# Optimization experiments

Hardware: AMD Instinct MI355X
Metric: run time of the kernel (lower is better)

The kernel has to match this reference:

```python
import jax, jax.numpy as jnp
import numpy as np

EPS = 1e-5

def layer_norm(x, w, b):
    mu = jnp.mean(x, axis=-1, keepdims=True)
    var = jnp.mean(jnp.square(x - mu), axis=-1, keepdims=True)
    return (x - mu) * jax.lax.rsqrt(var + EPS) * w + b

def setup_inputs() -> dict:
    key = jax.random.key(0)
    ks = jax.random.split(key, 12)
    B, T, C = 4, 2048, 1024
    s = lambda d: 1.0 / np.sqrt(d)
    return {
        "x":      jax.random.normal(ks[0], (B, T, C), dtype=jnp.float32),
        "w_attn": jax.random.normal(ks[1], (C, 3 * C), dtype=jnp.float32) * s(C),
        "b_attn": jnp.zeros((3 * C,), jnp.float32),
        "w_o":    jax.random.normal(ks[2], (C, C), dtype=jnp.float32) * s(C),
        "b_o":    jnp.zeros((C,), jnp.float32),
        "ln_w":   jnp.ones((C,), jnp.float32),
        "ln_b":   jnp.zeros((C,), jnp.float32),
        "w_fc1":  jax.random.normal(ks[3], (C, 4 * C), dtype=jnp.float32) * s(C),
        "b_fc1":  jnp.zeros((4 * C,), jnp.float32),
        "w_fc2":  jax.random.normal(ks[4], (4 * C, C), dtype=jnp.float32) * s(4 * C),
        "b_fc2":  jnp.zeros((C,), jnp.float32),
        "n_heads": 16,
    }

def reference(x, w_attn, b_attn, w_o, b_o, ln_w, ln_b, w_fc1, b_fc1, w_fc2, b_fc2, n_heads):
    B, T, C = x.shape
    H = n_heads
    Dh = C // H
    qkv = x @ w_attn + b_attn                      # [B,T,3C]
    q, k, v = jnp.split(qkv, 3, axis=-1)
    q = q.reshape(B, T, H, Dh).transpose(0, 2, 1, 3)  # [B,H,T,Dh]
    k = k.reshape(B, T, H, Dh).transpose(0, 2, 1, 3)
    v = v.reshape(B, T, H, Dh).transpose(0, 2, 1, 3)
    scores = jnp.einsum("bhtd,bhsd->bhts", q, k) / jnp.sqrt(jnp.float32(Dh))
    w = jax.nn.softmax(scores, axis=-1)            # no causal mask in source
    out = jnp.einsum("bhts,bhsd->bhtd", w, v)      # [B,H,T,Dh]
    out = out.transpose(0, 2, 1, 3).reshape(B, T, C)
    attn_out = out @ w_o + b_o
    x = x + attn_out
    h = layer_norm(x, ln_w, ln_b)
    h = jax.nn.gelu(h @ w_fc1 + b_fc1, approximate=False)
    h = h @ w_fc2 + b_fc2
    return x + h
```

## Files before the change

### kernel.cpp

```cpp
#include <hip/hip_runtime.h>
#include <hip/hip_bf16.h>
#include <math.h>
#include <stdint.h>

typedef __attribute__((ext_vector_type(8))) short s16x8;
typedef __attribute__((ext_vector_type(4))) float f32x4;
typedef __attribute__((ext_vector_type(4))) u_int32_t u32x4;
typedef unsigned int u32;
typedef unsigned short u16;

#define DEVINL __device__ __forceinline__
#define VMW(n) asm volatile("s_waitcnt vmcnt(" #n ")" ::: "memory")

DEVINL u16 f2bf(float f) {
    u32 b = __builtin_bit_cast(u32, f);
    u32 r = (b + 0x7fffu + ((b >> 16) & 1u)) >> 16;
    return (u16)r;
}

DEVINL float fexp2(float x) {
    float r;
    asm("v_exp_f32 %0, %1" : "=v"(r) : "v"(x));
    return r;
}

DEVINL u32 cvt_pk_bf16(float lo, float hi) {
    u32 r;
    asm("v_cvt_pk_bf16_f32 %0, %1, %2" : "=v"(r) : "v"(lo), "v"(hi));
    return r;
}

DEVINL void gload_lds16(const void* g, const void* l) {
    __builtin_amdgcn_global_load_lds(
        (const __attribute__((address_space(1))) u32*)(uintptr_t)g,
        (__attribute__((address_space(3))) u32*)(uintptr_t)l, 16, 0, 0);
}

__global__ __launch_bounds__(256)
void cvt_bf16_kernel(const float* __restrict__ in, u16* __restrict__ out, int n4)
{
    int i = blockIdx.x * 256 + threadIdx.x;
    const int stride = gridDim.x * 256;
    for (; i < n4; i += stride) {
        float4 v = ((const float4*)in)[i];
        ushort4 o;
        o.x = f2bf(v.x); o.y = f2bf(v.y); o.z = f2bf(v.z); o.w = f2bf(v.w);
        ((ushort4*)out)[i] = o;
    }
}

__global__ __launch_bounds__(256)
void transpose_cvt(const float* __restrict__ src, u16* __restrict__ dst, int R, int C)
{
    __shared__ float tile[64][65];
    const int t = threadIdx.x;
    const int c0 = blockIdx.x * 64, r0 = blockIdx.y * 64;
    const int rr = t >> 6;
    const int cc = t & 63;
    #pragma unroll
    for (int i = 0; i < 16; ++i)
        tile[i * 4 + rr][cc] = src[(size_t)(r0 + i * 4 + rr) * C + c0 + cc];
    __syncthreads();
    #pragma unroll
    for (int i = 0; i < 16; ++i) {
        int orow = i * 4 + rr;
        dst[(size_t)(c0 + orow) * R + r0 + cc] = f2bf(tile[cc][orow]);
    }
}

__global__ __launch_bounds__(256)
void vtrans_kernel(const u16* __restrict__ qkv, u16* __restrict__ vt)
{
    __shared__ u16 tile[64][68];
    const int t = threadIdx.x;
    const int st = blockIdx.x;
    const int bh = blockIdx.y;
    const int b = bh >> 4, h = bh & 15;
    const int s0 = st * 64;
    const int rr = t >> 6, cc = t & 63;
    const int sc = (cc & 32) | (((cc >> 2) & 3) << 3) | (((cc >> 4) & 1) << 2) | (cc & 3);
    #pragma unroll
    for (int i = 0; i < 16; ++i) {
        int s = i * 4 + rr;
        tile[s][cc] = qkv[(size_t)(b * 2048 + s0 + s) * 3072 + 2048 + h * 64 + cc];
    }
    __syncthreads();
    #pragma unroll
    for (int i = 0; i < 16; ++i) {
        int d = i * 4 + rr;
        vt[(size_t)(bh * 64 + d) * 2048 + s0 + sc] = tile[cc][d];
    }
}

template<int MODE, int QSC>
__global__ __launch_bounds__(512, 1)
void gemm3s(const u16* __restrict__ A, const u16* __restrict__ B,
            const float* __restrict__ bias, const float* __restrict__ resid,
            u16* __restrict__ obf, float* __restrict__ of32,
            int M, int N, int K)
{
    constexpr int ABYTES = 128 * 128;
    constexpr int BUF = ABYTES + 32768;
    extern __shared__ char lds[];

    const int t = threadIdx.x, lane = t & 63, w = t >> 6;
    const int wr = w >> 2, wc = w & 3, g = lane >> 4, lr = lane & 15;
    const int id = blockIdx.x;
    const int bm = (((id & 7) << 3) | ((id >> 3) & 7)) * 128;
    const int bn = (id >> 6) * 256;

    const int srow = t >> 3;
    const int scol = (((t & 7) ^ (srow & 7)) * 8);
    const u16* ag = A + (size_t)(bm + srow) * K + scol;
    const u16* bg = B + (size_t)(bn + srow) * K + scol;

    f32x4 acc[4][4] = {};

    auto STAGE = [&](int tt) {
        char* bb = lds + (tt % 3) * BUF;
        const size_t ko = (size_t)tt * 64;
        #pragma unroll
        for (int L = 0; L < 2; ++L)
            gload_lds16(ag + (size_t)L * 64 * K + ko, bb + L * 8192 + t * 16);
        #pragma unroll
        for (int L = 0; L < 4; ++L)
            gload_lds16(bg + (size_t)L * 64 * K + ko, bb + ABYTES + L * 8192 + t * 16);
    };

    const int NT = K >> 6;
    STAGE(0); STAGE(1);

    const int xr = (lr & 7) << 4;

    for (int tt = 0; tt < NT; ++tt) {
        if (tt < NT - 1) { VMW(6); } else { VMW(0); }
        __builtin_amdgcn_s_barrier();
        asm volatile("" ::: "memory");
        if (tt + 2 < NT) STAGE(tt + 2);

        const char* cbuf = lds + (tt % 3) * BUF;
        s16x8 af[4][2], bf4[4][2];
        #pragma unroll
        for (int mf = 0; mf < 4; ++mf) {
            const int arow = wr * 64 + mf * 16 + lr;
            #pragma unroll
            for (int ks = 0; ks < 2; ++ks)
                af[mf][ks] = *(const s16x8*)(cbuf + arow * 128 + ((ks * 64 + g * 16) ^ xr));
        }
        #pragma unroll
        for (int nf = 0; nf < 4; ++nf) {
            const int brow = wc * 64 + nf * 16 + lr;
            #pragma unroll
            for (int ks = 0; ks < 2; ++ks)
                bf4[nf][ks] = *(const s16x8*)(cbuf + ABYTES + brow * 128 + ((ks * 64 + g * 16) ^ xr));
        }
        __builtin_amdgcn_s_setprio(1);
        #pragma unroll
        for (int ks = 0; ks < 2; ++ks)
            #pragma unroll
            for (int mf = 0; mf < 4; ++mf)
                #pragma unroll
                for (int nf = 0; nf < 4; ++nf)
                    acc[mf][nf] = __builtin_amdgcn_mfma_f32_16x16x32_bf16(
                        af[mf][ks], bf4[nf][ks], acc[mf][nf], 0, 0, 0);
        __builtin_amdgcn_s_setprio(0);
    }

    #pragma unroll
    for (int mf = 0; mf < 4; ++mf) {
        const int rbase = bm + wr * 64 + mf * 16 + g * 4;
        #pragma unroll
        for (int nf = 0; nf < 4; ++nf) {
            const int col = bn + wc * 64 + nf * 16 + lr;
            const float bia = bias[col];
            #pragma unroll
            for (int b2 = 0; b2 < 4; ++b2) {
                const int r = rbase + b2;
                float v = acc[mf][nf][b2] + bia;
                if (QSC && col < 1024) v *= 0.18033688011112042f;
                if (MODE == 1) v = 0.5f * v * (1.0f + erff(v * 0.70710678118654752f));
                if (MODE == 2) {
                    v += resid[(size_t)r * N + col];
                    of32[(size_t)r * N + col] = v;
                } else {
                    obf[(size_t)r * N + col] = f2bf(v);
                }
            }
        }
    }
}

__global__ __launch_bounds__(512)
void attn_kernel(const u16* __restrict__ qkv, const u16* __restrict__ vt,
                 u16* __restrict__ attnb)
{
    __shared__ u16 Kls[2][4096];
    __shared__ u16 Vls[2][4096];
    const int t = threadIdx.x, lane = t & 63, w = t >> 6;
    const int g = lane >> 4, lr = lane & 15;
    const int wg = blockIdx.x;
    const int xcd = wg & 7, slot = wg >> 3;
    const int bh = xcd * 8 + (slot >> 4);
    const int qt = slot & 15;
    const int b = bh >> 4, h = bh & 15;

    const int srow = t >> 3;
    const int scol = (((t & 7) ^ (srow & 7)) * 8);
    const u16* kg = qkv + (size_t)(b * 2048 + srow) * 3072 + 1024 + h * 64 + scol;
    const u16* vg = vt + (size_t)(bh * 64 + srow) * 2048 + scol;

    gload_lds16(kg, &Kls[0][t * 8]);
    gload_lds16(vg, &Vls[0][t * 8]);

    const int qtok = b * 2048 + qt * 128 + w * 16 + lr;
    const u16* qp = qkv + (size_t)qtok * 3072 + h * 64;
    const s16x8 qf0 = *(const s16x8*)(qp + g * 8);
    const s16x8 qf1 = *(const s16x8*)(qp + 32 + g * 8);

    f32x4 o[4] = {};
    float psum = 0.f;
    const int xr = (lr & 7) * 8;

    for (int s = 0; s < 32; ++s) {
        const int cur = s & 1;
        __syncthreads();
        if (s + 1 < 32) {
            const size_t ko = (size_t)(s + 1) * 64;
            gload_lds16(kg + ko * 3072, &Kls[cur ^ 1][t * 8]);
            gload_lds16(vg + ko, &Vls[cur ^ 1][t * 8]);
        }

        f32x4 sv[4];
        #pragma unroll
        for (int n = 0; n < 4; ++n) {
            const int kr = (n * 16 + lr) * 64;
            const s16x8 k0v = *(const s16x8*)&Kls[cur][kr + ((g * 8) ^ xr)];
            const s16x8 k1v = *(const s16x8*)&Kls[cur][kr + ((32 + g * 8) ^ xr)];
            f32x4 z = {};
            z = __builtin_amdgcn_mfma_f32_16x16x32_bf16(k0v, qf0, z, 0, 0, 0);
            z = __builtin_amdgcn_mfma_f32_16x16x32_bf16(k1v, qf1, z, 0, 0, 0);
            sv[n] = z;
        }

        float p[4][4];
        #pragma unroll
        for (int n = 0; n < 4; ++n) {
            #pragma unroll
            for (int b2 = 0; b2 < 4; ++b2)
                p[n][b2] = fexp2(sv[n][b2]);
            psum += (p[n][0] + p[n][1]) + (p[n][2] + p[n][3]);
        }

        u32x4 pk0, pk1;
        pk0[0] = cvt_pk_bf16(p[0][0], p[0][1]);
        pk0[1] = cvt_pk_bf16(p[0][2], p[0][3]);
        pk0[2] = cvt_pk_bf16(p[1][0], p[1][1]);
        pk0[3] = cvt_pk_bf16(p[1][2], p[1][3]);
        pk1[0] = cvt_pk_bf16(p[2][0], p[2][1]);
        pk1[1] = cvt_pk_bf16(p[2][2], p[2][3]);
        pk1[2] = cvt_pk_bf16(p[3][0], p[3][1]);
        pk1[3] = cvt_pk_bf16(p[3][2], p[3][3]);
        const s16x8 pa0 = __builtin_bit_cast(s16x8, pk0);
        const s16x8 pa1 = __builtin_bit_cast(s16x8, pk1);

        #pragma unroll
        for (int n = 0; n < 4; ++n) {
            const int vr = (n * 16 + lr) * 64;
            const s16x8 v0 = *(const s16x8*)&Vls[cur][vr + ((g * 8) ^ xr)];
            const s16x8 v1 = *(const s16x8*)&Vls[cur][vr + ((32 + g * 8) ^ xr)];
            o[n] = __builtin_amdgcn_mfma_f32_16x16x32_bf16(pa0, v0, o[n], 0, 0, 0);
            o[n] = __builtin_amdgcn_mfma_f32_16x16x32_bf16(pa1, v1, o[n], 0, 0, 0);
        }
    }

    psum += __shfl_xor(psum, 16);
    psum += __shfl_xor(psum, 32);
    const int orow0 = b * 2048 + qt * 128 + w * 16 + g * 4;
    #pragma unroll
    for (int b2 = 0; b2 < 4; ++b2) {
        const float inv = 1.0f / __shfl(psum, g * 4 + b2);
        #pragma unroll
        for (int n = 0; n < 4; ++n)
            attnb[(size_t)(orow0 + b2) * 1024 + h * 64 + n * 16 + lr] = f2bf(o[n][b2] * inv);
    }
}

__global__ __launch_bounds__(256)
void ln_kernel(const float* __restrict__ x, const float* __restrict__ lw,
               const float* __restrict__ lb, u16* __restrict__ out)
{
    const int row = blockIdx.x;
    const int t = threadIdx.x;
    const float4 v = ((const float4*)(x + (size_t)row * 1024))[t];
    float s = v.x + v.y + v.z + v.w;
    float s2 = v.x * v.x + v.y * v.y + v.z * v.z + v.w * v.w;
    #pragma unroll
    for (int m = 32; m >= 1; m >>= 1) {
        s  += __shfl_xor(s, m);
        s2 += __shfl_xor(s2, m);
    }
    __shared__ float red[16];
    const int w = t >> 6, lane = t & 63;
    if (lane == 0) { red[w] = s; red[8 + w] = s2; }
    __syncthreads();
    s  = red[0] + red[1] + red[2] + red[3];
    s2 = red[8] + red[9] + red[10] + red[11];
    const float mu = s * (1.0f / 1024.0f);
    const float var = s2 * (1.0f / 1024.0f) - mu * mu;
    const float inv = rsqrtf(var + 1e-5f);
    const float4 wv = ((const float4*)lw)[t];
    const float4 bv = ((const float4*)lb)[t];
    ushort4 oo;
    oo.x = f2bf((v.x - mu) * inv * wv.x + bv.x);
    oo.y = f2bf((v.y - mu) * inv * wv.y + bv.y);
    oo.z = f2bf((v.z - mu) * inv * wv.z + bv.z);
    oo.w = f2bf((v.w - mu) * inv * wv.w + bv.w);
    ((ushort4*)(out + (size_t)row * 1024))[t] = oo;
}

extern "C" void kernel_launch(void* const* d_in, const int* in_sizes, int n_in,
                              void* d_out, int out_size, void* d_ws, size_t ws_size,
                              hipStream_t stream)
{
    const float* x      = (const float*)d_in[0];
    const float* w_attn = (const float*)d_in[1];
    const float* b_attn = (const float*)d_in[2];
    const float* w_o    = (const float*)d_in[3];
    const float* b_o    = (const float*)d_in[4];
    const float* ln_w   = (const float*)d_in[5];
    const float* ln_b   = (const float*)d_in[6];
    const float* w_fc1  = (const float*)d_in[7];
    const float* b_fc1  = (const float*)d_in[8];
    const float* w_fc2  = (const float*)d_in[9];
    const float* b_fc2  = (const float*)d_in[10];
    float* out = (float*)d_out;

    char* ws = (char*)d_ws;
    u16*   xb    = (u16*)(ws);
    u16*   wqkvT = (u16*)(ws + 16777216);
    u16*   woT   = (u16*)(ws + 23068672);
    u16*   w1T   = (u16*)(ws + 25165824);
    u16*   w2T   = (u16*)(ws + 33554432);
    float* x1    = (float*)(ws + 41943040);
    u16*   attnb = (u16*)(ws + 75497472);
    u16*   hb    = attnb;
    u16*   qkvb  = (u16*)(ws + 92274688);
    u16*   vtb   = qkvb + 25165824;
    u16*   h1    = qkvb;

    cvt_bf16_kernel<<<2048, 256, 0, stream>>>(x, xb, 8192 * 1024 / 4);
    transpose_cvt<<<dim3(48, 16), 256, 0, stream>>>(w_attn, wqkvT, 1024, 3072);
    transpose_cvt<<<dim3(16, 16), 256, 0, stream>>>(w_o,   woT,  1024, 1024);
    transpose_cvt<<<dim3(64, 16), 256, 0, stream>>>(w_fc1, w1T,  1024, 4096);
    transpose_cvt<<<dim3(16, 64), 256, 0, stream>>>(w_fc2, w2T,  4096, 1024);

    gemm3s<0, 1><<<768, 512, 147456, stream>>>(xb, wqkvT, b_attn, nullptr,
                                               qkvb, nullptr, 8192, 3072, 1024);
    vtrans_kernel<<<dim3(32, 64), 256, 0, stream>>>(qkvb, vtb);
    attn_kernel<<<1024, 512, 0, stream>>>(qkvb, vtb, attnb);
    gemm3s<2, 0><<<256, 512, 147456, stream>>>(attnb, woT, b_o, x,
                                               nullptr, x1, 8192, 1024, 1024);
    ln_kernel<<<8192, 256, 0, stream>>>(x1, ln_w, ln_b, hb);
    gemm3s<1, 0><<<1024, 512, 147456, stream>>>(hb, w1T, b_fc1, nullptr,
                                                h1, nullptr, 8192, 4096, 1024);
    gemm3s<2, 0><<<256, 512, 147456, stream>>>(h1, w2T, b_fc2, x1,
                                               nullptr, out, 8192, 1024, 4096);
}
```

Before: 412.6 us.

## Restructure GEMM into double-buffered phased MFMA loop with templated M tile

Replaces the triple-buffered GEMM with a double-buffered one that issues the next stage's loads before waiting. The inner loop is split into phases: A fragments for the next phase are read from LDS while the current MFMAs run, with a barrier between phases. The M tile becomes a template parameter, the FC1 GEMM uses 256-row tiles, and block swizzling is dropped in favour of a plain 2D grid. This lowers LDS use and register pressure and raises per-block reuse on FC1, at the cost of extra barriers, less prefetch depth and the loss of the L2-friendly block ordering.

```diff
diff --git a/kernel.cpp b/kernel.cpp
--- a/kernel.cpp
+++ b/kernel.cpp
@@ -92,61 +92,59 @@
     }
 }
 
-template<int MODE, int QSC>
+template<int BM, int MODE, int QSC>
 __global__ __launch_bounds__(512, 1)
-void gemm3s(const u16* __restrict__ A, const u16* __restrict__ B,
+void gemmph(const u16* __restrict__ A, const u16* __restrict__ B,
             const float* __restrict__ bias, const float* __restrict__ resid,
             u16* __restrict__ obf, float* __restrict__ of32,
             int M, int N, int K)
 {
-    constexpr int ABYTES = 128 * 128;
+    constexpr int MF = BM / 32;
+    constexpr int NPH = MF / 2;
+    constexpr int AL = BM / 64;
+    constexpr int ABYTES = BM * 128;
     constexpr int BUF = ABYTES + 32768;
     extern __shared__ char lds[];
 
     const int t = threadIdx.x, lane = t & 63, w = t >> 6;
     const int wr = w >> 2, wc = w & 3, g = lane >> 4, lr = lane & 15;
-    const int id = blockIdx.x;
-    const int bm = (((id & 7) << 3) | ((id >> 3) & 7)) * 128;
-    const int bn = (id >> 6) * 256;
+    const int bm = blockIdx.x * BM, bn = blockIdx.y * 256;
 
     const int srow = t >> 3;
     const int scol = (((t & 7) ^ (srow & 7)) * 8);
     const u16* ag = A + (size_t)(bm + srow) * K + scol;
     const u16* bg = B + (size_t)(bn + srow) * K + scol;
 
-    f32x4 acc[4][4] = {};
+    f32x4 acc[MF][4] = {};
 
     auto STAGE = [&](int tt) {
-        char* bb = lds + (tt % 3) * BUF;
+        char* bb = lds + (tt & 1) * BUF;
         const size_t ko = (size_t)tt * 64;
         #pragma unroll
-        for (int L = 0; L < 2; ++L)
+        for (int L = 0; L < AL; ++L)
             gload_lds16(ag + (size_t)L * 64 * K + ko, bb + L * 8192 + t * 16);
         #pragma unroll
         for (int L = 0; L < 4; ++L)
             gload_lds16(bg + (size_t)L * 64 * K + ko, bb + ABYTES + L * 8192 + t * 16);
     };
 
+    const int xr = (lr & 7) << 4;
     const int NT = K >> 6;
-    STAGE(0); STAGE(1);
-
-    const int xr = (lr & 7) << 4;
+
+    STAGE(0);
 
     for (int tt = 0; tt < NT; ++tt) {
-        if (tt < NT - 1) { VMW(6); } else { VMW(0); }
+        const char* cbuf = lds + (tt & 1) * BUF;
+
+        if (tt + 1 < NT) {
+            STAGE(tt + 1);
+            if constexpr (BM == 256) { VMW(8); } else { VMW(6); }
+        } else {
+            VMW(0);
+        }
         __builtin_amdgcn_s_barrier();
-        asm volatile("" ::: "memory");
-        if (tt + 2 < NT) STAGE(tt + 2);
-
-        const char* cbuf = lds + (tt % 3) * BUF;
-        s16x8 af[4][2], bf4[4][2];
-        #pragma unroll
-        for (int mf = 0; mf < 4; ++mf) {
-            const int arow = wr * 64 + mf * 16 + lr;
-            #pragma unroll
-            for (int ks = 0; ks < 2; ++ks)
-                af[mf][ks] = *(const s16x8*)(cbuf + arow * 128 + ((ks * 64 + g * 16) ^ xr));
-        }
+
+        s16x8 bf4[4][2];
         #pragma unroll
         for (int nf = 0; nf < 4; ++nf) {
             const int brow = wc * 64 + nf * 16 + lr;
@@ -154,21 +152,51 @@
             for (int ks = 0; ks < 2; ++ks)
                 bf4[nf][ks] = *(const s16x8*)(cbuf + ABYTES + brow * 128 + ((ks * 64 + g * 16) ^ xr));
         }
-        __builtin_amdgcn_s_setprio(1);
-        #pragma unroll
-        for (int ks = 0; ks < 2; ++ks)
-            #pragma unroll
-            for (int mf = 0; mf < 4; ++mf)
+        s16x8 afr[2][2];
+        #pragma unroll
+        for (int mi = 0; mi < 2; ++mi) {
+            const int arow = wr * (BM / 2) + mi * 16 + lr;
+            #pragma unroll
+            for (int ks = 0; ks < 2; ++ks)
+                afr[mi][ks] = *(const s16x8*)(cbuf + arow * 128 + ((ks * 64 + g * 16) ^ xr));
+        }
+
+        #pragma unroll
+        for (int p = 0; p < NPH; ++p) {
+            s16x8 nxt[2][2];
+            if (p + 1 < NPH) {
                 #pragma unroll
-                for (int nf = 0; nf < 4; ++nf)
-                    acc[mf][nf] = __builtin_amdgcn_mfma_f32_16x16x32_bf16(
-                        af[mf][ks], bf4[nf][ks], acc[mf][nf], 0, 0, 0);
-        __builtin_amdgcn_s_setprio(0);
-    }
-
-    #pragma unroll
-    for (int mf = 0; mf < 4; ++mf) {
-        const int rbase = bm + wr * 64 + mf * 16 + g * 4;
+                for (int mi = 0; mi < 2; ++mi) {
+                    const int arow = wr * (BM / 2) + ((p + 1) * 2 + mi) * 16 + lr;
+                    #pragma unroll
+                    for (int ks = 0; ks < 2; ++ks)
+                        nxt[mi][ks] = *(const s16x8*)(cbuf + arow * 128 + ((ks * 64 + g * 16) ^ xr));
+                }
+            }
+            __builtin_amdgcn_s_setprio(1);
+            #pragma unroll
+            for (int ks = 0; ks < 2; ++ks)
+                #pragma unroll
+                for (int mi = 0; mi < 2; ++mi)
+                    #pragma unroll
+                    for (int nf = 0; nf < 4; ++nf)
+                        acc[p * 2 + mi][nf] = __builtin_amdgcn_mfma_f32_16x16x32_bf16(
+                            afr[mi][ks], bf4[nf][ks], acc[p * 2 + mi][nf], 0, 0, 0);
+            __builtin_amdgcn_s_setprio(0);
+            __builtin_amdgcn_s_barrier();
+            if (p + 1 < NPH) {
+                #pragma unroll
+                for (int mi = 0; mi < 2; ++mi)
+                    #pragma unroll
+                    for (int ks = 0; ks < 2; ++ks)
+                        afr[mi][ks] = nxt[mi][ks];
+            }
+        }
+    }
+
+    #pragma unroll
+    for (int mf = 0; mf < MF; ++mf) {
+        const int rbase = bm + wr * (BM / 2) + mf * 16 + g * 4;
         #pragma unroll
         for (int nf = 0; nf < 4; ++nf) {
             const int col = bn + wc * 64 + nf * 16 + lr;
@@ -354,15 +382,15 @@
     transpose_cvt<<<dim3(64, 16), 256, 0, stream>>>(w_fc1, w1T,  1024, 4096);
     transpose_cvt<<<dim3(16, 64), 256, 0, stream>>>(w_fc2, w2T,  4096, 1024);
 
-    gemm3s<0, 1><<<768, 512, 147456, stream>>>(xb, wqkvT, b_attn, nullptr,
-                                               qkvb, nullptr, 8192, 3072, 1024);
+    gemmph<128, 0, 1><<<dim3(64, 12), 512, 98304, stream>>>(xb, wqkvT, b_attn, nullptr,
+                                                            qkvb, nullptr, 8192, 3072, 1024);
     vtrans_kernel<<<dim3(32, 64), 256, 0, stream>>>(qkvb, vtb);
     attn_kernel<<<1024, 512, 0, stream>>>(qkvb, vtb, attnb);
-    gemm3s<2, 0><<<256, 512, 147456, stream>>>(attnb, woT, b_o, x,
-                                               nullptr, x1, 8192, 1024, 1024);
+    gemmph<128, 2, 0><<<dim3(64, 4), 512, 98304, stream>>>(attnb, woT, b_o, x,
+                                                           nullptr, x1, 8192, 1024, 1024);
     ln_kernel<<<8192, 256, 0, stream>>>(x1, ln_w, ln_b, hb);
-    gemm3s<1, 0><<<1024, 512, 147456, stream>>>(hb, w1T, b_fc1, nullptr,
-                                                h1, nullptr, 8192, 4096, 1024);
-    gemm3s<2, 0><<<256, 512, 147456, stream>>>(h1, w2T, b_fc2, x1,
-                                               nullptr, out, 8192, 1024, 4096);
-}
+    gemmph<256, 1, 0><<<dim3(32, 16), 512, 131072, stream>>>(hb, w1T, b_fc1, nullptr,
+                                                             h1, nullptr, 8192, 4096, 1024);
+    gemmph<128, 2, 0><<<dim3(64, 4), 512, 98304, stream>>>(h1, w2T, b_fc2, x1,
+                                                           nullptr, out, 8192, 1024, 4096);
+}
```

Measured after the change: 413.0 us. Within noise of the previous version (+0.1%).
